# Kernel tuning notes

Hardware: AMD Instinct MI355X
Metric: run time of the kernel (lower is better)

The kernel has to match this reference:

```python
import jax, jax.numpy as jnp
import numpy as np
from jax import lax

B, C, H, W = 4, 128, 64, 64
GC = 32        # branch channels = C * branch_ratio
DI = 64        # SS2D d_inner = 2 * GC (expand=2)
DT_RANK = 2    # ceil(GC / 16)


def _conv(x, w, pad, dilation=1, groups=1):
    return lax.conv_general_dilated(x, w, (1, 1), [(pad, pad), (pad, pad)],
                                    rhs_dilation=(dilation, dilation),
                                    feature_group_count=groups,
                                    dimension_numbers=('NCHW', 'OIHW', 'NCHW'))


def _bn(x, g, b, m, v):
    # inference-mode BatchNorm2d
    s = g / jnp.sqrt(v + 1e-5)
    return x * s[None, :, None, None] + (b - m * s)[None, :, None, None]


def _selective_scan(u, delta, A, Bm, Cm, D, dbias):
    # u, delta: (B,K,Di,L); A: (K,Di,N); Bm,Cm: (B,K,N,L); D,dbias: (K,Di)
    delta = jax.nn.softplus(delta + dbias[None, :, :, None])
    Bsz, K, Di, L = u.shape
    N = A.shape[-1]

    def step(h, inp):
        dt, bt, ct, ut = inp  # dt,ut: (B,K,Di); bt,ct: (B,K,N)
        h = jnp.exp(dt[..., None] * A) * h + (dt * ut)[..., None] * bt[:, :, None, :]
        return h, jnp.einsum('bkdn,bkn->bkd', h, ct)

    xs = (jnp.moveaxis(delta, -1, 0), jnp.moveaxis(Bm, -1, 0),
          jnp.moveaxis(Cm, -1, 0), jnp.moveaxis(u, -1, 0))
    _, ys = lax.scan(step, jnp.zeros((Bsz, K, Di, N), u.dtype), xs)
    return jnp.moveaxis(ys, 0, -1) + u * D[None, :, :, None]


def _ss2d(x, in_w, cw, cb, xp_w, dt_w, dt_b, A_log, Dp, ln_g, ln_b, out_w):
    # VMamba SS2D on NCHW input
    Bsz, Cc, Hh, Ww = x.shape
    di = in_w.shape[0] // 2
    dc = cw.shape[-1]
    xz = jnp.einsum('bchw,ec->behw', x, in_w)          # in_proj (bias=False)
    xi, z = jnp.split(xz, 2, axis=1)
    xc = jax.nn.silu(_conv(xi, cw, (dc - 1) // 2, groups=di) + cb[None, :, None, None])
    L = Hh * Ww
    xf = xc.reshape(Bsz, di, L)
    xt = xc.transpose(0, 1, 3, 2).reshape(Bsz, di, L)
    x2 = jnp.stack([xf, xt], 1)
    xs4 = jnp.concatenate([x2, jnp.flip(x2, -1)], 1)   # (B,4,di,L) cross-scan
    x_dbl = jnp.einsum('bkdl,kcd->bkcl', xs4, xp_w)
    r = dt_w.shape[-1]
    N = A_log.shape[-1]
    dts = jnp.einsum('bkrl,kdr->bkdl', x_dbl[:, :, :r], dt_w)
    Bs = x_dbl[:, :, r:r + N]
    Cs = x_dbl[:, :, r + N:]
    A = -jnp.exp(A_log).reshape(4, di, N)
    oy = _selective_scan(xs4, dts, A, Bs, Cs, Dp.reshape(4, di), dt_b)
    inv = jnp.flip(oy[:, 2:4], -1)
    wh = oy[:, 1].reshape(Bsz, di, Ww, Hh).transpose(0, 1, 3, 2).reshape(Bsz, di, L)
    iwh = inv[:, 1].reshape(Bsz, di, Ww, Hh).transpose(0, 1, 3, 2).reshape(Bsz, di, L)
    y = (oy[:, 0] + inv[:, 0] + wh + iwh).transpose(0, 2, 1).reshape(Bsz, Hh, Ww, di)
    mu = y.mean(-1, keepdims=True)
    y = (y - mu) * lax.rsqrt(((y - mu) ** 2).mean(-1, keepdims=True) + 1e-5) * ln_g + ln_b
    y = y * jax.nn.silu(z.transpose(0, 2, 3, 1))
    return jnp.einsum('bhwd,cd->bchw', y, out_w)


def _gcss2d(x, in_w, cw, cb, xp_w, dt_w, dt_b, A_log, Dp, ln_g, ln_b, out_w, pw, bg, bb, bm, bv):
    s = _ss2d(x, in_w, cw, cb, xp_w, dt_w, dt_b, A_log, Dp, ln_g, ln_b, out_w)
    # AdaptiveAvgPool2d(1) + bilinear upsample of a 1x1 map == broadcast
    pool = jnp.broadcast_to(x.mean((2, 3), keepdims=True), s.shape)
    return jax.nn.relu(_bn(_conv(jnp.concatenate([s, pool], 1), pw, 0), bg, bb, bm, bv))


def _forward(x, conv1_w, conv1_bn_g, conv1_bn_b, conv1_bn_m, conv1_bn_v,
             ss2_in_proj_w, ss2_conv_w, ss2_conv_b, ss2_x_proj_w, ss2_dt_w, ss2_dt_b,
             ss2_A_log, ss2_D, ss2_ln_g, ss2_ln_b, ss2_out_proj_w,
             g2_proj_w, g2_bn_g, g2_bn_b, g2_bn_m, g2_bn_v,
             conv3_w,
             ss4_in_proj_w, ss4_conv_w, ss4_conv_b, ss4_x_proj_w, ss4_dt_w, ss4_dt_b,
             ss4_A_log, ss4_D, ss4_ln_g, ss4_ln_b, ss4_out_proj_w,
             g4_proj_w, g4_bn_g, g4_bn_b, g4_bn_m, g4_bn_v,
             gp_w, proj_w, proj_bn_g, proj_bn_b, proj_bn_m, proj_bn_v,
             ca_w1, ca_b1, ca_w2, ca_b2, sa_w):
    Cc = x.shape[1]
    x1, x2, x3, x4 = jnp.split(x, [Cc - 3 * GC, Cc - 2 * GC, Cc - GC], axis=1)
    out1 = jax.nn.relu(_bn(_conv(x1, conv1_w, 1), conv1_bn_g, conv1_bn_b, conv1_bn_m, conv1_bn_v))
    out2 = _gcss2d(x2, ss2_in_proj_w, ss2_conv_w, ss2_conv_b, ss2_x_proj_w, ss2_dt_w,
                   ss2_dt_b, ss2_A_log, ss2_D, ss2_ln_g, ss2_ln_b, ss2_out_proj_w,
                   g2_proj_w, g2_bn_g, g2_bn_b, g2_bn_m, g2_bn_v)
    out3 = jax.nn.relu(_conv(x3 + x1, conv3_w, 12, dilation=12))
    out4 = _gcss2d(x4 + x2, ss4_in_proj_w, ss4_conv_w, ss4_conv_b, ss4_x_proj_w, ss4_dt_w,
                   ss4_dt_b, ss4_A_log, ss4_D, ss4_ln_g, ss4_ln_b, ss4_out_proj_w,
                   g4_proj_w, g4_bn_g, g4_bn_b, g4_bn_m, g4_bn_v)
    fused = jnp.concatenate([out1, out2, out3, out4], 1)
    gf = jax.nn.relu(_conv(x.mean((2, 3), keepdims=True), gp_w, 0))
    gf = jnp.broadcast_to(gf, fused.shape)
    y = jnp.concatenate([fused, gf], 1)
    y = x + jax.nn.relu(_bn(_conv(y, proj_w, 0), proj_bn_g, proj_bn_b, proj_bn_m, proj_bn_v))
    # RCSA (dropout is identity in eval)
    ca = jax.nn.sigmoid(
        _conv(jax.nn.relu(_conv(y.mean((2, 3), keepdims=True), ca_w1, 0)
                          + ca_b1[None, :, None, None]), ca_w2, 0)
        + ca_b2[None, :, None, None])
    sa = jax.nn.sigmoid(_conv(y, sa_w, 3))
    return y * (ca * sa) + y


def setup_inputs():
    key = jax.random.key(0)
    ctr = [0]

    def rn(shape, s=0.1):
        ctr[0] += 1
        return s * jax.random.normal(jax.random.fold_in(key, ctr[0]), shape, jnp.float32)

    def alog(n):
        # VMamba A init: log(1..N) per (direction*d_inner) row
        return jnp.tile(jnp.log(jnp.arange(1, n + 1, dtype=jnp.float32))[None], (4 * DI, 1))

    return dict(
        x=rn((B, C, H, W), 1.0),
        conv1_w=rn((GC, GC, 3, 3)),
        conv1_bn_g=jnp.ones(GC), conv1_bn_b=jnp.zeros(GC),
        conv1_bn_m=jnp.zeros(GC), conv1_bn_v=jnp.ones(GC),
        ss2_in_proj_w=rn((2 * DI, GC)),
        ss2_conv_w=rn((DI, 1, 3, 3)), ss2_conv_b=rn((DI,)),
        ss2_x_proj_w=rn((4, DT_RANK + 2 * 8, DI)),
        ss2_dt_w=rn((4, DI, DT_RANK)), ss2_dt_b=rn((4, DI)),
        ss2_A_log=alog(8), ss2_D=jnp.ones(4 * DI),
        ss2_ln_g=jnp.ones(DI), ss2_ln_b=jnp.zeros(DI),
        ss2_out_proj_w=rn((GC, DI)),
        g2_proj_w=rn((GC, 2 * GC, 1, 1)),
        g2_bn_g=jnp.ones(GC), g2_bn_b=jnp.zeros(GC), g2_bn_m=jnp.zeros(GC), g2_bn_v=jnp.ones(GC),
        conv3_w=rn((GC, GC, 3, 3)),
        ss4_in_proj_w=rn((2 * DI, GC)),
        ss4_conv_w=rn((DI, 1, 7, 7)), ss4_conv_b=rn((DI,)),
        ss4_x_proj_w=rn((4, DT_RANK + 2 * 24, DI)),
        ss4_dt_w=rn((4, DI, DT_RANK)), ss4_dt_b=rn((4, DI)),
        ss4_A_log=alog(24), ss4_D=jnp.ones(4 * DI),
        ss4_ln_g=jnp.ones(DI), ss4_ln_b=jnp.zeros(DI),
        ss4_out_proj_w=rn((GC, DI)),
        g4_proj_w=rn((GC, 2 * GC, 1, 1)),
        g4_bn_g=jnp.ones(GC), g4_bn_b=jnp.zeros(GC), g4_bn_m=jnp.zeros(GC), g4_bn_v=jnp.ones(GC),
        gp_w=rn((C, C, 1, 1)),
        proj_w=rn((C, 2 * C, 1, 1)),
        proj_bn_g=jnp.ones(C), proj_bn_b=jnp.zeros(C),
        proj_bn_m=jnp.zeros(C), proj_bn_v=jnp.ones(C),
        ca_w1=rn((C // 16, C, 1, 1)), ca_b1=jnp.zeros(C // 16),
        ca_w2=rn((C, C // 16, 1, 1)), ca_b2=jnp.zeros(C),
        sa_w=rn((1, C, 7, 7)),
    )


def reference(x, conv1_w, conv1_bn_g, conv1_bn_b, conv1_bn_m, conv1_bn_v,
              ss2_in_proj_w, ss2_conv_w, ss2_conv_b, ss2_x_proj_w, ss2_dt_w, ss2_dt_b,
              ss2_A_log, ss2_D, ss2_ln_g, ss2_ln_b, ss2_out_proj_w,
              g2_proj_w, g2_bn_g, g2_bn_b, g2_bn_m, g2_bn_v,
              conv3_w,
              ss4_in_proj_w, ss4_conv_w, ss4_conv_b, ss4_x_proj_w, ss4_dt_w, ss4_dt_b,
              ss4_A_log, ss4_D, ss4_ln_g, ss4_ln_b, ss4_out_proj_w,
              g4_proj_w, g4_bn_g, g4_bn_b, g4_bn_m, g4_bn_v,
              gp_w, proj_w, proj_bn_g, proj_bn_b, proj_bn_m, proj_bn_v,
              ca_w1, ca_b1, ca_w2, ca_b2, sa_w):
    return _forward(x, conv1_w, conv1_bn_g, conv1_bn_b, conv1_bn_m, conv1_bn_v,
                    ss2_in_proj_w, ss2_conv_w, ss2_conv_b, ss2_x_proj_w, ss2_dt_w, ss2_dt_b,
                    ss2_A_log, ss2_D, ss2_ln_g, ss2_ln_b, ss2_out_proj_w,
                    g2_proj_w, g2_bn_g, g2_bn_b, g2_bn_m, g2_bn_v,
                    conv3_w,
                    ss4_in_proj_w, ss4_conv_w, ss4_conv_b, ss4_x_proj_w, ss4_dt_w, ss4_dt_b,
                    ss4_A_log, ss4_D, ss4_ln_g, ss4_ln_b, ss4_out_proj_w,
                    g4_proj_w, g4_bn_g, g4_bn_b, g4_bn_m, g4_bn_v,
                    gp_w, proj_w, proj_bn_g, proj_bn_b, proj_bn_m, proj_bn_v,
                    ca_w1, ca_b1, ca_w2, ca_b2, sa_w)
```

## Files before the change

kernel.cpp:

```cpp
#include <hip/hip_runtime.h>
#include <math.h>

#define BB 4
#define CCH 128
#define LL 4096
#define LOG2E 1.44269504088896340736f

__device__ __forceinline__ float exp2fast(float x) {
    float r; asm("v_exp_f32 %0, %1" : "=v"(r) : "v"(x)); return r;
}
__device__ __forceinline__ float softplusf(float x) {
    return x > 20.f ? x : log1pf(expf(x));
}
__device__ __forceinline__ float sigmf(float x) {
    return 1.f / (1.f + expf(-x));
}

__device__ __forceinline__ int dirmap(int k, int l) {
    if (k == 0) return l;
    if (k == 1) return ((l & 63) << 6) | (l >> 6);
    if (k == 2) return LL - 1 - l;
    int j = LL - 1 - l; return ((j & 63) << 6) | (j >> 6);
}

__global__ void k_prepA(const float* __restrict__ Alog2, const float* __restrict__ Alog4,
                        float* __restrict__ A2_2, float* __restrict__ A2_4) {
    int i = blockIdx.x * 256 + threadIdx.x;
    if (i < 4 * 64 * 8)  A2_2[i] = -expf(Alog2[i]) * LOG2E;
    if (i < 4 * 64 * 24) A2_4[i] = -expf(Alog4[i]) * LOG2E;
}

__global__ void k_addgroups(const float* __restrict__ x, float* __restrict__ x13, float* __restrict__ x42) {
    int i = blockIdx.x * 256 + threadIdx.x;
    int l = i & (LL - 1); int c = (i >> 12) & 31; int b = i >> 17;
    const float* xb = x + (size_t)b * CCH * LL;
    x13[i] = xb[(64 + c) * LL + l] + xb[(0 + c) * LL + l];
    x42[i] = xb[(96 + c) * LL + l] + xb[(32 + c) * LL + l];
}

__global__ void k_pool(const float* __restrict__ src, float* __restrict__ dst) {
    int bc = blockIdx.x;
    const float* p = src + (size_t)bc * LL;
    float s = 0.f;
    for (int i = threadIdx.x; i < LL; i += 256) s += p[i];
    for (int m = 32; m >= 1; m >>= 1) s += __shfl_xor(s, m, 64);
    __shared__ float ws[4];
    if ((threadIdx.x & 63) == 0) ws[threadIdx.x >> 6] = s;
    __syncthreads();
    if (threadIdx.x == 0) dst[bc] = (ws[0] + ws[1] + ws[2] + ws[3]) * (1.f / LL);
}

__global__ __launch_bounds__(256) void k_conv1L(const float* __restrict__ x,
                        const float* __restrict__ w1,
                        const float* __restrict__ g, const float* __restrict__ bt,
                        const float* __restrict__ m, const float* __restrict__ v,
                        float* __restrict__ out1) {
    __shared__ float t[32][3][66];
    int b = blockIdx.x >> 6, h = blockIdx.x & 63;
    int lane = threadIdx.x & 63, wv = threadIdx.x >> 6;
    const float* xb = x + (size_t)b * CCH * LL;
    for (int i = threadIdx.x; i < 192; i += 256) {
        int ci = i / 6, rem = i % 6;
        t[ci][rem >> 1][(rem & 1) ? 65 : 0] = 0.f;
    }
    for (int i = threadIdx.x; i < 6144; i += 256) {
        int ci = i / 192, rem = i % 192;
        int r = rem >> 6, col = rem & 63;
        int hh = h + r - 1;
        t[ci][r][col + 1] = ((unsigned)hh < 64u) ? xb[ci * LL + hh * 64 + col] : 0.f;
    }
    __syncthreads();
    float a[8];
    #pragma unroll
    for (int j = 0; j < 8; j++) a[j] = 0.f;
    for (int ci = 0; ci < 32; ci++) {
        #pragma unroll
        for (int r = 0; r < 3; r++) {
            float v0 = t[ci][r][lane];
            float v1 = t[ci][r][lane + 1];
            float v2 = t[ci][r][lane + 2];
            #pragma unroll
            for (int j = 0; j < 8; j++) {
                const float* wp = w1 + ((wv * 8 + j) * 32 + ci) * 9 + r * 3;
                a[j] = fmaf(wp[0], v0, fmaf(wp[1], v1, fmaf(wp[2], v2, a[j])));
            }
        }
    }
    #pragma unroll
    for (int j = 0; j < 8; j++) {
        int co = wv * 8 + j;
        float sc = g[co] * rsqrtf(v[co] + 1e-5f);
        float bs = bt[co] - m[co] * sc;
        out1[(size_t)(b * 32 + co) * LL + h * 64 + lane] = fmaxf(fmaf(a[j], sc, bs), 0.f);
    }
}

__global__ __launch_bounds__(256) void k_conv3L(const float* __restrict__ x13,
                        const float* __restrict__ w3, float* __restrict__ out3) {
    __shared__ float t[32][3][88];
    int b = blockIdx.x >> 6, h = blockIdx.x & 63;
    int lane = threadIdx.x & 63, wv = threadIdx.x >> 6;
    const float* xb = x13 + (size_t)b * 32 * LL;
    for (int i = threadIdx.x; i < 2304; i += 256) {
        int ci = i / 72, rem = i % 72;
        int r = rem / 24, cz = rem % 24;
        t[ci][r][(cz < 12) ? cz : (cz + 64)] = 0.f;
    }
    for (int i = threadIdx.x; i < 6144; i += 256) {
        int ci = i / 192, rem = i % 192;
        int r = rem >> 6, col = rem & 63;
        int hh = h + (r - 1) * 12;
        t[ci][r][col + 12] = ((unsigned)hh < 64u) ? xb[ci * LL + hh * 64 + col] : 0.f;
    }
    __syncthreads();
    float a[8];
    #pragma unroll
    for (int j = 0; j < 8; j++) a[j] = 0.f;
    for (int ci = 0; ci < 32; ci++) {
        #pragma unroll
        for (int r = 0; r < 3; r++) {
            float v0 = t[ci][r][lane];
            float v1 = t[ci][r][lane + 12];
            float v2 = t[ci][r][lane + 24];
            #pragma unroll
            for (int j = 0; j < 8; j++) {
                const float* wp = w3 + ((wv * 8 + j) * 32 + ci) * 9 + r * 3;
                a[j] = fmaf(wp[0], v0, fmaf(wp[1], v1, fmaf(wp[2], v2, a[j])));
            }
        }
    }
    #pragma unroll
    for (int j = 0; j < 8; j++) {
        int co = wv * 8 + j;
        out3[(size_t)(b * 32 + co) * LL + h * 64 + lane] = fmaxf(a[j], 0.f);
    }
}

__global__ __launch_bounds__(256) void k_s1(const float* __restrict__ src, int bstride, int coff,
                     const float* __restrict__ in_w,
                     float* __restrict__ xiT, float* __restrict__ zT) {
    int blk = blockIdx.x;
    int l0 = (blk & 63) * 64; int b = blk >> 6;
    int lq = threadIdx.x & 63; int esub = threadIdx.x >> 6;
    __shared__ float xin[32][64];
    __shared__ float xit[64][65];
    __shared__ float zt[64][65];
    for (int i = threadIdx.x; i < 32 * 64; i += 256) {
        int c = i >> 6, q = i & 63;
        xin[c][q] = src[(size_t)b * bstride + (size_t)(coff + c) * LL + l0 + q];
    }
    __syncthreads();
    for (int it = 0; it < 32; it++) {
        int e = esub * 32 + it;
        const float* wr = in_w + e * 32;
        float acc = 0.f;
        #pragma unroll 8
        for (int c = 0; c < 32; c++) acc += wr[c] * xin[c][lq];
        if (e < 64) xit[lq][e] = acc;
        else        zt[lq][e - 64] = acc;
    }
    __syncthreads();
    for (int i = threadIdx.x; i < 64 * 64; i += 256) {
        int q = i >> 6, d = i & 63;
        size_t st = ((size_t)b * LL + l0 + q) * 64 + d;
        xiT[st] = xit[q][d];
        zT[st]  = zt[q][d];
    }
}

template<int K>
__global__ __launch_bounds__(256) void k_s2(const float* __restrict__ xiT, const float* __restrict__ cw,
                     const float* __restrict__ cb, float* __restrict__ xcT) {
    __shared__ float wl[64 * K * K];
    for (int j = threadIdx.x; j < 64 * K * K; j += 256) wl[j] = cw[j];
    __syncthreads();
    int i = blockIdx.x * 256 + threadIdx.x;
    int d = i & 63; int l = (i >> 6) & (LL - 1); int b = i >> 18;
    int h = l >> 6, wx = l & 63;
    const int P = (K - 1) / 2;
    const float* xb = xiT + (size_t)b * LL * 64;
    const float* wp = wl + d * K * K;
    float acc = cb[d];
    #pragma unroll
    for (int kh = 0; kh < K; kh++) {
        int hh = h + kh - P; if ((unsigned)hh >= 64u) continue;
        #pragma unroll
        for (int kw = 0; kw < K; kw++) {
            int w2 = wx + kw - P; if ((unsigned)w2 >= 64u) continue;
            acc += wp[kh * K + kw] * xb[(size_t)(hh * 64 + w2) * 64 + d];
        }
    }
    xcT[i] = acc / (1.f + expf(-acc));
}

template<int N>
__global__ __launch_bounds__(256) void k_s3(const float* __restrict__ xcT, const float* __restrict__ xp_w,
                     float* __restrict__ r01, float* __restrict__ Bsb, float* __restrict__ Csb) {
    const int CD = 2 + 2 * N;
    int blk = blockIdx.x;
    int lt = blk & 255; int k = (blk >> 8) & 3; int b = blk >> 10;
    int l0 = lt * 16; int bk = b * 4 + k;
    __shared__ float xt[64][17];
    __shared__ float xp[CD * 64];
    __shared__ float accs[CD][16];
    for (int i = threadIdx.x; i < 64 * 16; i += 256) {
        int dd = i & 63, lq = i >> 6;
        xt[dd][lq] = xcT[((size_t)b * LL + dirmap(k, l0 + lq)) * 64 + dd];
    }
    for (int i = threadIdx.x; i < CD * 64; i += 256) xp[i] = xp_w[(size_t)k * CD * 64 + i];
    __syncthreads();
    for (int o = threadIdx.x; o < CD * 16; o += 256) {
        int cc = o >> 4, lq = o & 15;
        const float* wr = &xp[cc * 64];
        float acc = 0.f;
        #pragma unroll 8
        for (int dd = 0; dd < 64; dd++) acc += wr[dd] * xt[dd][lq];
        accs[cc][lq] = acc;
    }
    __syncthreads();
    for (int i = threadIdx.x; i < 32; i += 256) {
        int lq = i >> 1, j = i & 1;
        r01[((size_t)bk * LL + l0 + lq) * 2 + j] = accs[j][lq];
    }
    for (int i = threadIdx.x; i < 16 * N; i += 256) {
        int lq = i / N, n = i - lq * N;
        Bsb[((size_t)bk * LL + l0 + lq) * N + n] = accs[2 + n][lq];
        Csb[((size_t)bk * LL + l0 + lq) * N + n] = accs[2 + N + n][lq];
    }
}

template<int N>
__global__ __launch_bounds__(256) void k_scanA(
    const float* __restrict__ r01, const float* __restrict__ Bs,
    const float* __restrict__ xcT, const float* __restrict__ A2,
    const float* __restrict__ dtw, const float* __restrict__ dtb,
    float* __restrict__ Pp, float* __restrict__ Hl) {
    int bk = blockIdx.x >> 5; int c = (blockIdx.x & 31) * 4 + (threadIdx.x >> 6);
    int d = threadIdx.x & 63;
    int k = bk & 3, b = bk >> 2;
    float w0 = dtw[(k * 64 + d) * 2], w1 = dtw[(k * 64 + d) * 2 + 1], bd = dtb[k * 64 + d];
    float a2[N], h[N], P[N];
    #pragma unroll
    for (int n = 0; n < N; n++) { a2[n] = A2[(k * 64 + d) * N + n]; h[n] = 0.f; P[n] = 1.f; }
    const float2* rp  = (const float2*)(r01 + (size_t)bk * LL * 2);
    const float4* Bp4 = (const float4*)(Bs + (size_t)bk * LL * N);
    const float*  xb  = xcT + (size_t)b * LL * 64;
    int l0 = c * 32;
    for (int t = 0; t < 32; t++) {
        int l = l0 + t;
        float2 rv = rp[l];
        float dt = softplusf(fmaf(rv.x, w0, fmaf(rv.y, w1, bd)));
        float du = dt * xb[(size_t)dirmap(k, l) * 64 + d];
        #pragma unroll
        for (int n4 = 0; n4 < N / 4; n4++) {
            float4 bv = Bp4[(size_t)l * (N / 4) + n4];
            float bvs[4] = {bv.x, bv.y, bv.z, bv.w};
            #pragma unroll
            for (int j = 0; j < 4; j++) {
                int n = n4 * 4 + j;
                float a = exp2fast(dt * a2[n]);
                P[n] *= a;
                h[n] = fmaf(a, h[n], du * bvs[j]);
            }
        }
    }
    size_t o = (size_t)(bk * 128 + c) * N * 64 + d;
    #pragma unroll
    for (int n = 0; n < N; n++) { Pp[o + n * 64] = P[n]; Hl[o + n * 64] = h[n]; }
}

template<int N>
__global__ void k_scanB(const float* __restrict__ Pp, float* __restrict__ Hl) {
    int g = blockIdx.x * 256 + threadIdx.x;
    if (g >= 16 * N * 64) return;
    int d = g & 63; int n = (g >> 6) % N; int bk = g / (N * 64);
    float acc = 0.f;
    for (int c = 0; c < 128; c++) {
        size_t o = (size_t)(bk * 128 + c) * N * 64 + n * 64 + d;
        float Pv = Pp[o], Hv = Hl[o];
        Hl[o] = acc;
        acc = fmaf(Pv, acc, Hv);
    }
}

template<int N>
__global__ __launch_bounds__(256) void k_scanC(
    const float* __restrict__ r01, const float* __restrict__ Bs,
    const float* __restrict__ Cs, const float* __restrict__ xcT,
    const float* __restrict__ A2, const float* __restrict__ dtw,
    const float* __restrict__ dtb, const float* __restrict__ Hin,
    float* __restrict__ yrT) {
    int bk = blockIdx.x >> 5; int c = (blockIdx.x & 31) * 4 + (threadIdx.x >> 6);
    int d = threadIdx.x & 63;
    int k = bk & 3, b = bk >> 2;
    float w0 = dtw[(k * 64 + d) * 2], w1 = dtw[(k * 64 + d) * 2 + 1], bd = dtb[k * 64 + d];
    float a2[N], h[N];
    size_t o = (size_t)(bk * 128 + c) * N * 64 + d;
    #pragma unroll
    for (int n = 0; n < N; n++) { a2[n] = A2[(k * 64 + d) * N + n]; h[n] = Hin[o + n * 64]; }
    const float2* rp  = (const float2*)(r01 + (size_t)bk * LL * 2);
    const float4* Bp4 = (const float4*)(Bs + (size_t)bk * LL * N);
    const float4* Cp4 = (const float4*)(Cs + (size_t)bk * LL * N);
    const float*  xb  = xcT + (size_t)b * LL * 64;
    float* yo = yrT + (size_t)(k * BB + b) * LL * 64 + d;
    int l0 = c * 32;
    for (int t = 0; t < 32; t++) {
        int l = l0 + t;
        float2 rv = rp[l];
        float dt = softplusf(fmaf(rv.x, w0, fmaf(rv.y, w1, bd)));
        int lm = dirmap(k, l);
        float du = dt * xb[(size_t)lm * 64 + d];
        float y = 0.f;
        #pragma unroll
        for (int n4 = 0; n4 < N / 4; n4++) {
            float4 bv = Bp4[(size_t)l * (N / 4) + n4];
            float4 cv = Cp4[(size_t)l * (N / 4) + n4];
            float bvs[4] = {bv.x, bv.y, bv.z, bv.w};
            float cvs[4] = {cv.x, cv.y, cv.z, cv.w};
            #pragma unroll
            for (int j = 0; j < 4; j++) {
                int n = n4 * 4 + j;
                float a = exp2fast(dt * a2[n]);
                h[n] = fmaf(a, h[n], du * bvs[j]);
                y = fmaf(h[n], cvs[j], y);
            }
        }
        yo[(size_t)lm * 64] = y;
    }
}

__global__ __launch_bounds__(256) void k_combine(const float* __restrict__ yrT, const float* __restrict__ xcT,
                          const float* __restrict__ zT, const float* __restrict__ Dp,
                          const float* __restrict__ ln_g, const float* __restrict__ ln_b,
                          const float* __restrict__ out_w, float* __restrict__ sbuf) {
    int blk = blockIdx.x;
    int l0 = (blk & 127) * 32; int b = blk >> 7;
    int tid = threadIdx.x;
    __shared__ float yt[32][65];
    __shared__ float yg[32][65];
    __shared__ float muS[32], rsS[32];
    const size_t DS = (size_t)BB * LL * 64;
    for (int i = tid; i < 2048; i += 256) {
        int d = i & 63, q = i >> 6;
        size_t st = ((size_t)b * LL + l0 + q) * 64 + d;
        float yv = yrT[st] + yrT[DS + st] + yrT[2 * DS + st] + yrT[3 * DS + st];
        float sd = Dp[d] + Dp[64 + d] + Dp[128 + d] + Dp[192 + d];
        yt[q][d] = fmaf(xcT[st], sd, yv);
    }
    __syncthreads();
    {
        int q = tid >> 3, sub = tid & 7;
        float s = 0.f, sq = 0.f;
        #pragma unroll
        for (int j = 0; j < 8; j++) {
            float vv = yt[q][sub * 8 + j]; s += vv; sq = fmaf(vv, vv, sq);
        }
        #pragma unroll
        for (int m = 1; m < 8; m <<= 1) {
            s += __shfl_xor(s, m, 64); sq += __shfl_xor(sq, m, 64);
        }
        if (sub == 0) {
            float mm = s * (1.f / 64.f);
            muS[q] = mm;
            rsS[q] = rsqrtf(fmaf(sq, 1.f / 64.f, -mm * mm) + 1e-5f);
        }
    }
    __syncthreads();
    for (int i = tid; i < 2048; i += 256) {
        int d = i & 63, q = i >> 6;
        float gn = fmaf((yt[q][d] - muS[q]) * rsS[q], ln_g[d], ln_b[d]);
        float z = zT[((size_t)b * LL + l0 + q) * 64 + d];
        yg[q][d] = gn * z / (1.f + expf(-z));
    }
    __syncthreads();
    for (int i = tid; i < 32 * 32; i += 256) {
        int e = i >> 5, q = i & 31;
        const float* wr = out_w + e * 64;
        float acc = 0.f;
        #pragma unroll 8
        for (int d = 0; d < 64; d++) acc += wr[d] * yg[q][d];
        sbuf[((size_t)b * 32 + e) * LL + l0 + q] = acc;
    }
}

__global__ __launch_bounds__(256) void k_gtail(const float* __restrict__ sbuf, const float* __restrict__ pw,
                        const float* __restrict__ gfpool, int poolOff, int poolOff2,
                        const float* __restrict__ g, const float* __restrict__ bt,
                        const float* __restrict__ m, const float* __restrict__ v,
                        float* __restrict__ out) {
    int i = blockIdx.x * 256 + threadIdx.x;
    int l4 = i & 1023; int co = (i >> 10) & 31; int b = i >> 15;
    int l = l4 << 2;
    const float* pwr = pw + co * 64;
    float pacc = 0.f;
    #pragma unroll 8
    for (int c = 0; c < 32; c++) {
        float pv = gfpool[b * 128 + poolOff + c];
        if (poolOff2 >= 0) pv += gfpool[b * 128 + poolOff2 + c];
        pacc = fmaf(pwr[32 + c], pv, pacc);
    }
    float a0 = pacc, a1 = pacc, a2 = pacc, a3 = pacc;
    const float* sb = sbuf + (size_t)b * 32 * LL + l;
    #pragma unroll 8
    for (int c = 0; c < 32; c++) {
        float4 sv = *(const float4*)(sb + (size_t)c * LL);
        float wk = pwr[c];
        a0 = fmaf(wk, sv.x, a0);
        a1 = fmaf(wk, sv.y, a1);
        a2 = fmaf(wk, sv.z, a2);
        a3 = fmaf(wk, sv.w, a3);
    }
    float sc = g[co] * rsqrtf(v[co] + 1e-5f);
    float bs = bt[co] - m[co] * sc;
    float4 o;
    o.x = fmaxf(fmaf(a0, sc, bs), 0.f);
    o.y = fmaxf(fmaf(a1, sc, bs), 0.f);
    o.z = fmaxf(fmaf(a2, sc, bs), 0.f);
    o.w = fmaxf(fmaf(a3, sc, bs), 0.f);
    *(float4*)(out + (size_t)(b * 32 + co) * LL + l) = o;
}

__global__ void k_gf(const float* __restrict__ gfpool, const float* __restrict__ gp_w,
                     const float* __restrict__ proj_w, float* __restrict__ gf, float* __restrict__ pgf) {
    __shared__ float gfl[4][128];
    int t = threadIdx.x;
    int b = t >> 7, e = t & 127;
    float acc = 0.f;
    for (int c = 0; c < 128; c++) acc += gp_w[e * 128 + c] * gfpool[b * 128 + c];
    acc = fmaxf(acc, 0.f);
    gf[b * 128 + e] = acc; gfl[b][e] = acc;
    __syncthreads();
    float a2 = 0.f;
    for (int c = 0; c < 128; c++) a2 += proj_w[e * 256 + 128 + c] * gfl[b][c];
    pgf[b * 128 + e] = a2;
}

__global__ __launch_bounds__(256) void k_proj(const float* __restrict__ x,
                       const float* __restrict__ o1, const float* __restrict__ o2,
                       const float* __restrict__ o3, const float* __restrict__ o4,
                       const float* __restrict__ proj_w, const float* __restrict__ pgf,
                       const float* __restrict__ g, const float* __restrict__ bt,
                       const float* __restrict__ m, const float* __restrict__ v,
                       float* __restrict__ ybuf) {
    int i = blockIdx.x * 256 + threadIdx.x;
    int l4 = i & 1023; int co = (i >> 10) & 127; int b = i >> 17;
    int l = l4 << 2;
    const float* wr = proj_w + co * 256;
    float pg = pgf[b * 128 + co];
    float a0 = pg, a1 = pg, a2 = pg, a3 = pg;
    size_t ob = (size_t)b * 32 * LL + l;
    #pragma unroll 8
    for (int c = 0; c < 32; c++) {
        float4 vv = *(const float4*)(o1 + ob + (size_t)c * LL);
        float wk = wr[c];
        a0 = fmaf(wk, vv.x, a0); a1 = fmaf(wk, vv.y, a1);
        a2 = fmaf(wk, vv.z, a2); a3 = fmaf(wk, vv.w, a3);
    }
    #pragma unroll 8
    for (int c = 0; c < 32; c++) {
        float4 vv = *(const float4*)(o2 + ob + (size_t)c * LL);
        float wk = wr[32 + c];
        a0 = fmaf(wk, vv.x, a0); a1 = fmaf(wk, vv.y, a1);
        a2 = fmaf(wk, vv.z, a2); a3 = fmaf(wk, vv.w, a3);
    }
    #pragma unroll 8
    for (int c = 0; c < 32; c++) {
        float4 vv = *(const float4*)(o3 + ob + (size_t)c * LL);
        float wk = wr[64 + c];
        a0 = fmaf(wk, vv.x, a0); a1 = fmaf(wk, vv.y, a1);
        a2 = fmaf(wk, vv.z, a2); a3 = fmaf(wk, vv.w, a3);
    }
    #pragma unroll 8
    for (int c = 0; c < 32; c++) {
        float4 vv = *(const float4*)(o4 + ob + (size_t)c * LL);
        float wk = wr[96 + c];
        a0 = fmaf(wk, vv.x, a0); a1 = fmaf(wk, vv.y, a1);
        a2 = fmaf(wk, vv.z, a2); a3 = fmaf(wk, vv.w, a3);
    }
    float sc = g[co] * rsqrtf(v[co] + 1e-5f);
    float bs = bt[co] - m[co] * sc;
    float4 xv = *(const float4*)(x + (size_t)(b * 128 + co) * LL + l);
    float4 o;
    o.x = xv.x + fmaxf(fmaf(a0, sc, bs), 0.f);
    o.y = xv.y + fmaxf(fmaf(a1, sc, bs), 0.f);
    o.z = xv.z + fmaxf(fmaf(a2, sc, bs), 0.f);
    o.w = xv.w + fmaxf(fmaf(a3, sc, bs), 0.f);
    *(float4*)(ybuf + (size_t)(b * 128 + co) * LL + l) = o;
}

__global__ void k_ca(const float* __restrict__ ypool, const float* __restrict__ w1,
                     const float* __restrict__ b1, const float* __restrict__ w2,
                     const float* __restrict__ b2, float* __restrict__ ca) {
    int b = blockIdx.x; int t = threadIdx.x;
    __shared__ float ym[128]; __shared__ float r1[8];
    ym[t] = ypool[b * 128 + t];
    __syncthreads();
    if (t < 8) {
        float a = b1[t];
        for (int c = 0; c < 128; c++) a += w1[t * 128 + c] * ym[c];
        r1[t] = fmaxf(a, 0.f);
    }
    __syncthreads();
    float a = b2[t];
    #pragma unroll
    for (int i2 = 0; i2 < 8; i2++) a += w2[t * 8 + i2] * r1[i2];
    ca[b * 128 + t] = sigmf(a);
}

__global__ __launch_bounds__(256) void k_sa_part(const float* __restrict__ ybuf, const float* __restrict__ sw,
                     float* __restrict__ pa) {
    __shared__ float wlds[16 * 49];
    __shared__ float rows[4][7][70];
    __shared__ float part[4][64];
    int cg = blockIdx.x & 7; int h = (blockIdx.x >> 3) & 63; int b = blockIdx.x >> 9;
    int lane = threadIdx.x & 63, wv = threadIdx.x >> 6;
    for (int i = threadIdx.x; i < 16 * 49; i += 256) wlds[i] = sw[cg * 16 * 49 + i];
    if (lane < 3) {
        #pragma unroll
        for (int r = 0; r < 7; r++) { rows[wv][r][lane] = 0.f; rows[wv][r][67 + lane] = 0.f; }
    }
    __syncthreads();
    float acc = 0.f;
    for (int it = 0; it < 4; it++) {
        int lc = it * 4 + wv; int c = cg * 16 + lc;
        const float* yp = ybuf + ((size_t)b * 128 + c) * LL;
        #pragma unroll
        for (int r = 0; r < 7; r++) {
            int hh = h + r - 3;
            rows[wv][r][3 + lane] = ((unsigned)hh < 64u) ? yp[hh * 64 + lane] : 0.f;
        }
        __syncthreads();
        const float* wp = wlds + lc * 49;
        #pragma unroll
        for (int kh = 0; kh < 7; kh++) {
            #pragma unroll
            for (int kw = 0; kw < 7; kw++) {
                acc = fmaf(wp[kh * 7 + kw], rows[wv][kh][lane + kw], acc);
            }
        }
        __syncthreads();
    }
    part[wv][lane] = acc;
    __syncthreads();
    if (threadIdx.x < 64) {
        float a = part[0][threadIdx.x] + part[1][threadIdx.x]
                + part[2][threadIdx.x] + part[3][threadIdx.x];
        pa[(size_t)cg * (BB * LL) + (size_t)b * LL + h * 64 + threadIdx.x] = a;
    }
}

__global__ void k_sared(const float* __restrict__ pa, float* __restrict__ sa) {
    int i = blockIdx.x * 256 + threadIdx.x;
    float s = 0.f;
    #pragma unroll
    for (int g = 0; g < 8; g++) s += pa[(size_t)g * (BB * LL) + i];
    sa[i] = sigmf(s);
}

__global__ void k_final(const float* __restrict__ ybuf, const float* __restrict__ ca,
                        const float* __restrict__ sa, float* __restrict__ out) {
    int i = blockIdx.x * 256 + threadIdx.x;
    int l = i & (LL - 1); int co = (i >> 12) & 127; int b = i >> 19;
    float y = ybuf[i];
    out[i] = y * (1.f + ca[b * 128 + co] * sa[b * 4096 + l]);
}

extern "C" void kernel_launch(void* const* d_in, const int* in_sizes, int n_in,
                              void* d_out, int out_size, void* d_ws, size_t ws_size,
                              hipStream_t stream) {
    const float* x        = (const float*)d_in[0];
    const float* conv1_w  = (const float*)d_in[1];
    const float* c1g = (const float*)d_in[2], *c1b = (const float*)d_in[3];
    const float* c1m = (const float*)d_in[4], *c1v = (const float*)d_in[5];
    const float* s2_inw   = (const float*)d_in[6];
    const float* s2_cw    = (const float*)d_in[7];
    const float* s2_cb    = (const float*)d_in[8];
    const float* s2_xpw   = (const float*)d_in[9];
    const float* s2_dtw   = (const float*)d_in[10];
    const float* s2_dtb   = (const float*)d_in[11];
    const float* s2_Alog  = (const float*)d_in[12];
    const float* s2_D     = (const float*)d_in[13];
    const float* s2_lng   = (const float*)d_in[14];
    const float* s2_lnb   = (const float*)d_in[15];
    const float* s2_outw  = (const float*)d_in[16];
    const float* g2_pw    = (const float*)d_in[17];
    const float* g2g = (const float*)d_in[18], *g2b = (const float*)d_in[19];
    const float* g2m = (const float*)d_in[20], *g2v = (const float*)d_in[21];
    const float* conv3_w  = (const float*)d_in[22];
    const float* s4_inw   = (const float*)d_in[23];
    const float* s4_cw    = (const float*)d_in[24];
    const float* s4_cb    = (const float*)d_in[25];
    const float* s4_xpw   = (const float*)d_in[26];
    const float* s4_dtw   = (const float*)d_in[27];
    const float* s4_dtb   = (const float*)d_in[28];
    const float* s4_Alog  = (const float*)d_in[29];
    const float* s4_D     = (const float*)d_in[30];
    const float* s4_lng   = (const float*)d_in[31];
    const float* s4_lnb   = (const float*)d_in[32];
    const float* s4_outw  = (const float*)d_in[33];
    const float* g4_pw    = (const float*)d_in[34];
    const float* g4g = (const float*)d_in[35], *g4b = (const float*)d_in[36];
    const float* g4m = (const float*)d_in[37], *g4v = (const float*)d_in[38];
    const float* gp_w     = (const float*)d_in[39];
    const float* proj_w   = (const float*)d_in[40];
    const float* pjg = (const float*)d_in[41], *pjb = (const float*)d_in[42];
    const float* pjm = (const float*)d_in[43], *pjv = (const float*)d_in[44];
    const float* ca_w1 = (const float*)d_in[45], *ca_b1 = (const float*)d_in[46];
    const float* ca_w2 = (const float*)d_in[47], *ca_b2 = (const float*)d_in[48];
    const float* sa_w  = (const float*)d_in[49];
    float* out = (float*)d_out;
    float* w = (float*)d_ws;

    const size_t o_out1 = 0;
    const size_t o_out2 = 524288;
    const size_t o_out3 = 1048576;
    const size_t o_out4 = 1572864;
    const size_t o_x42  = 2097152;
    const size_t o_gfp  = 2621440;
    const size_t o_gf   = 2621952;
    const size_t o_pgf  = 2622464;
    const size_t o_ypool= 2622976;
    const size_t o_ca   = 2623488;
    const size_t o_A2   = 2624000;
    const size_t o_A4   = 2626048;
    const size_t o_S    = 2632192;
    const size_t o_x13  = o_S;
    const size_t o_xiT  = o_S;
    const size_t o_Pp   = o_S;
    const size_t o_yrT  = o_S;
    const size_t o_ybuf = o_S;
    const size_t o_sa   = o_S + 2097152;
    const size_t o_sap  = o_S + 2113536;
    const size_t o_zT   = o_S + 4194304;
    const size_t o_xcT  = o_zT + 1048576;
    const size_t o_r01  = o_xcT + 1048576;
    const size_t o_Bs   = o_r01 + 131072;
    const size_t o_sbuf = o_Bs;
    const size_t o_Cs   = o_Bs + 1572864;
    const size_t o_Hl   = o_Cs + 1572864;

    dim3 b256(256);
    k_prepA<<<24, b256, 0, stream>>>(s2_Alog, s4_Alog, w + o_A2, w + o_A4);
    k_addgroups<<<2048, b256, 0, stream>>>(x, w + o_x13, w + o_x42);
    k_pool<<<512, b256, 0, stream>>>(x, w + o_gfp);
    k_conv1L<<<256, b256, 0, stream>>>(x, conv1_w, c1g, c1b, c1m, c1v, w + o_out1);
    k_conv3L<<<256, b256, 0, stream>>>(w + o_x13, conv3_w, w + o_out3);

    {
        const int N = 8;
        k_s1<<<256, b256, 0, stream>>>(x, CCH * LL, 32, s2_inw, w + o_xiT, w + o_zT);
        k_s2<3><<<4096, b256, 0, stream>>>(w + o_xiT, s2_cw, s2_cb, w + o_xcT);
        k_s3<N><<<4096, b256, 0, stream>>>(w + o_xcT, s2_xpw, w + o_r01, w + o_Bs, w + o_Cs);
        k_scanA<N><<<512, b256, 0, stream>>>(w + o_r01, w + o_Bs, w + o_xcT, w + o_A2,
                                             s2_dtw, s2_dtb, w + o_Pp, w + o_Hl);
        k_scanB<N><<<(16 * N * 64 + 255) / 256, b256, 0, stream>>>(w + o_Pp, w + o_Hl);
        k_scanC<N><<<512, b256, 0, stream>>>(w + o_r01, w + o_Bs, w + o_Cs, w + o_xcT,
                                             w + o_A2, s2_dtw, s2_dtb, w + o_Hl, w + o_yrT);
        k_combine<<<512, b256, 0, stream>>>(w + o_yrT, w + o_xcT, w + o_zT, s2_D,
                                            s2_lng, s2_lnb, s2_outw, w + o_sbuf);
        k_gtail<<<512, b256, 0, stream>>>(w + o_sbuf, g2_pw, w + o_gfp, 32, -1,
                                          g2g, g2b, g2m, g2v, w + o_out2);
    }
    {
        const int N = 24;
        k_s1<<<256, b256, 0, stream>>>(w + o_x42, 32 * LL, 0, s4_inw, w + o_xiT, w + o_zT);
        k_s2<7><<<4096, b256, 0, stream>>>(w + o_xiT, s4_cw, s4_cb, w + o_xcT);
        k_s3<N><<<4096, b256, 0, stream>>>(w + o_xcT, s4_xpw, w + o_r01, w + o_Bs, w + o_Cs);
        k_scanA<N><<<512, b256, 0, stream>>>(w + o_r01, w + o_Bs, w + o_xcT, w + o_A4,
                                             s4_dtw, s4_dtb, w + o_Pp, w + o_Hl);
        k_scanB<N><<<(16 * N * 64 + 255) / 256, b256, 0, stream>>>(w + o_Pp, w + o_Hl);
        k_scanC<N><<<512, b256, 0, stream>>>(w + o_r01, w + o_Bs, w + o_Cs, w + o_xcT,
                                             w + o_A4, s4_dtw, s4_dtb, w + o_Hl, w + o_yrT);
        k_combine<<<512, b256, 0, stream>>>(w + o_yrT, w + o_xcT, w + o_zT, s4_D,
                                            s4_lng, s4_lnb, s4_outw, w + o_sbuf);
        k_gtail<<<512, b256, 0, stream>>>(w + o_sbuf, g4_pw, w + o_gfp, 96, 32,
                                          g4g, g4b, g4m, g4v, w + o_out4);
    }

    k_gf<<<1, dim3(512), 0, stream>>>(w + o_gfp, gp_w, proj_w, w + o_gf, w + o_pgf);
    k_proj<<<2048, b256, 0, stream>>>(x, w + o_out1, w + o_out2, w + o_out3, w + o_out4,
                                      proj_w, w + o_pgf, pjg, pjb, pjm, pjv, w + o_ybuf);
    k_pool<<<512, b256, 0, stream>>>(w + o_ybuf, w + o_ypool);
    k_ca<<<4, dim3(128), 0, stream>>>(w + o_ypool, ca_w1, ca_b1, ca_w2, ca_b2, w + o_ca);
    k_sa_part<<<2048, b256, 0, stream>>>(w + o_ybuf, sa_w, w + o_sap);
    k_sared<<<64, b256, 0, stream>>>(w + o_sap, w + o_sa);
    k_final<<<8192, b256, 0, stream>>>(w + o_ybuf, w + o_ca, w + o_sa, out);
}
```

Before: 697.0 us.

## Split scan state dimension across waves and stage B/C/dt in shared memory

The chunked selective-scan kernels now give each block a single 32-step chunk and split the N state dimension across the four waves, each handling N/4 states. The grid therefore grows fourfold and per-thread register arrays shrink. Softplus of dt and dt*u are computed once per chunk into shared memory, and B/C rows are staged in LDS. Partial y sums are reduced across waves through shared memory before the global store. The carry-propagation kernel also prefetches the next chunk's values. The cost is extra barriers and LDS traffic in exchange for more parallelism and occupancy.

```diff
diff --git a/kernel.cpp b/kernel.cpp
--- a/kernel.cpp
+++ b/kernel.cpp
@@ -235,38 +235,52 @@
     const float* __restrict__ xcT, const float* __restrict__ A2,
     const float* __restrict__ dtw, const float* __restrict__ dtb,
     float* __restrict__ Pp, float* __restrict__ Hl) {
-    int bk = blockIdx.x >> 5; int c = (blockIdx.x & 31) * 4 + (threadIdx.x >> 6);
-    int d = threadIdx.x & 63;
+    const int N4 = N / 4;
+    __shared__ float2 dd2[32][64];
+    __shared__ float lb[32 * N];
+    int bk = blockIdx.x >> 7; int c = blockIdx.x & 127;
     int k = bk & 3, b = bk >> 2;
-    float w0 = dtw[(k * 64 + d) * 2], w1 = dtw[(k * 64 + d) * 2 + 1], bd = dtb[k * 64 + d];
-    float a2[N], h[N], P[N];
-    #pragma unroll
-    for (int n = 0; n < N; n++) { a2[n] = A2[(k * 64 + d) * N + n]; h[n] = 0.f; P[n] = 1.f; }
-    const float2* rp  = (const float2*)(r01 + (size_t)bk * LL * 2);
-    const float4* Bp4 = (const float4*)(Bs + (size_t)bk * LL * N);
-    const float*  xb  = xcT + (size_t)b * LL * 64;
+    int tid = threadIdx.x;
+    int d = tid & 63, wv = tid >> 6;
     int l0 = c * 32;
+    const float* Bp = Bs + ((size_t)bk * LL + l0) * N;
+    for (int i = tid; i < 32 * N; i += 256) lb[i] = Bp[i];
+    {
+        float w0 = dtw[(k * 64 + d) * 2], w1 = dtw[(k * 64 + d) * 2 + 1], bd = dtb[k * 64 + d];
+        const float2* rp = (const float2*)(r01 + (size_t)bk * LL * 2);
+        const float* xb = xcT + (size_t)b * LL * 64;
+        #pragma unroll
+        for (int j = 0; j < 8; j++) {
+            int t = wv * 8 + j;
+            float2 rv = rp[l0 + t];
+            float u = xb[(size_t)dirmap(k, l0 + t) * 64 + d];
+            float dt = softplusf(fmaf(rv.x, w0, fmaf(rv.y, w1, bd)));
+            dd2[t][d] = make_float2(dt, dt * u);
+        }
+    }
+    __syncthreads();
+    float a2[N4], h[N4], P[N4];
+    #pragma unroll
+    for (int n = 0; n < N4; n++) {
+        a2[n] = A2[(k * 64 + d) * N + wv * N4 + n];
+        h[n] = 0.f; P[n] = 1.f;
+    }
     for (int t = 0; t < 32; t++) {
-        int l = l0 + t;
-        float2 rv = rp[l];
-        float dt = softplusf(fmaf(rv.x, w0, fmaf(rv.y, w1, bd)));
-        float du = dt * xb[(size_t)dirmap(k, l) * 64 + d];
-        #pragma unroll
-        for (int n4 = 0; n4 < N / 4; n4++) {
-            float4 bv = Bp4[(size_t)l * (N / 4) + n4];
-            float bvs[4] = {bv.x, bv.y, bv.z, bv.w};
-            #pragma unroll
-            for (int j = 0; j < 4; j++) {
-                int n = n4 * 4 + j;
-                float a = exp2fast(dt * a2[n]);
-                P[n] *= a;
-                h[n] = fmaf(a, h[n], du * bvs[j]);
-            }
+        float2 dv = dd2[t][d];
+        const float* bl = &lb[t * N + wv * N4];
+        #pragma unroll
+        for (int n = 0; n < N4; n++) {
+            float a = exp2fast(dv.x * a2[n]);
+            P[n] *= a;
+            h[n] = fmaf(a, h[n], dv.y * bl[n]);
         }
     }
     size_t o = (size_t)(bk * 128 + c) * N * 64 + d;
     #pragma unroll
-    for (int n = 0; n < N; n++) { Pp[o + n * 64] = P[n]; Hl[o + n * 64] = h[n]; }
+    for (int n = 0; n < N4; n++) {
+        Pp[o + (size_t)(wv * N4 + n) * 64] = P[n];
+        Hl[o + (size_t)(wv * N4 + n) * 64] = h[n];
+    }
 }
 
 template<int N>
@@ -274,12 +288,17 @@
     int g = blockIdx.x * 256 + threadIdx.x;
     if (g >= 16 * N * 64) return;
     int d = g & 63; int n = (g >> 6) % N; int bk = g / (N * 64);
+    const size_t stride = (size_t)N * 64;
+    size_t o = (size_t)bk * 128 * stride + n * 64 + d;
     float acc = 0.f;
+    float Pv = Pp[o], Hv = Hl[o];
     for (int c = 0; c < 128; c++) {
-        size_t o = (size_t)(bk * 128 + c) * N * 64 + n * 64 + d;
-        float Pv = Pp[o], Hv = Hl[o];
+        float Pn = 0.f, Hn = 0.f;
+        if (c < 127) { Pn = Pp[o + stride]; Hn = Hl[o + stride]; }
         Hl[o] = acc;
         acc = fmaf(Pv, acc, Hv);
+        Pv = Pn; Hv = Hn;
+        o += stride;
     }
 }
 
@@ -290,42 +309,64 @@
     const float* __restrict__ A2, const float* __restrict__ dtw,
     const float* __restrict__ dtb, const float* __restrict__ Hin,
     float* __restrict__ yrT) {
-    int bk = blockIdx.x >> 5; int c = (blockIdx.x & 31) * 4 + (threadIdx.x >> 6);
-    int d = threadIdx.x & 63;
+    const int N4 = N / 4;
+    __shared__ float2 dd2[32][64];
+    __shared__ float lb[32 * N];
+    __shared__ float lc[32 * N];
+    __shared__ float yacc[4][8][64];
+    int bk = blockIdx.x >> 7; int c = blockIdx.x & 127;
     int k = bk & 3, b = bk >> 2;
-    float w0 = dtw[(k * 64 + d) * 2], w1 = dtw[(k * 64 + d) * 2 + 1], bd = dtb[k * 64 + d];
-    float a2[N], h[N];
+    int tid = threadIdx.x;
+    int d = tid & 63, wv = tid >> 6;
+    int l0 = c * 32;
+    const float* Bp = Bs + ((size_t)bk * LL + l0) * N;
+    const float* Cp = Cs + ((size_t)bk * LL + l0) * N;
+    for (int i = tid; i < 32 * N; i += 256) { lb[i] = Bp[i]; lc[i] = Cp[i]; }
+    {
+        float w0 = dtw[(k * 64 + d) * 2], w1 = dtw[(k * 64 + d) * 2 + 1], bd = dtb[k * 64 + d];
+        const float2* rp = (const float2*)(r01 + (size_t)bk * LL * 2);
+        const float* xb = xcT + (size_t)b * LL * 64;
+        #pragma unroll
+        for (int j = 0; j < 8; j++) {
+            int t = wv * 8 + j;
+            float2 rv = rp[l0 + t];
+            float u = xb[(size_t)dirmap(k, l0 + t) * 64 + d];
+            float dt = softplusf(fmaf(rv.x, w0, fmaf(rv.y, w1, bd)));
+            dd2[t][d] = make_float2(dt, dt * u);
+        }
+    }
+    float a2[N4], h[N4];
     size_t o = (size_t)(bk * 128 + c) * N * 64 + d;
     #pragma unroll
-    for (int n = 0; n < N; n++) { a2[n] = A2[(k * 64 + d) * N + n]; h[n] = Hin[o + n * 64]; }
-    const float2* rp  = (const float2*)(r01 + (size_t)bk * LL * 2);
-    const float4* Bp4 = (const float4*)(Bs + (size_t)bk * LL * N);
-    const float4* Cp4 = (const float4*)(Cs + (size_t)bk * LL * N);
-    const float*  xb  = xcT + (size_t)b * LL * 64;
-    float* yo = yrT + (size_t)(k * BB + b) * LL * 64 + d;
-    int l0 = c * 32;
-    for (int t = 0; t < 32; t++) {
-        int l = l0 + t;
-        float2 rv = rp[l];
-        float dt = softplusf(fmaf(rv.x, w0, fmaf(rv.y, w1, bd)));
-        int lm = dirmap(k, l);
-        float du = dt * xb[(size_t)lm * 64 + d];
-        float y = 0.f;
-        #pragma unroll
-        for (int n4 = 0; n4 < N / 4; n4++) {
-            float4 bv = Bp4[(size_t)l * (N / 4) + n4];
-            float4 cv = Cp4[(size_t)l * (N / 4) + n4];
-            float bvs[4] = {bv.x, bv.y, bv.z, bv.w};
-            float cvs[4] = {cv.x, cv.y, cv.z, cv.w};
+    for (int n = 0; n < N4; n++) {
+        a2[n] = A2[(k * 64 + d) * N + wv * N4 + n];
+        h[n] = Hin[o + (size_t)(wv * N4 + n) * 64];
+    }
+    __syncthreads();
+    float* yo = yrT + (size_t)(k * BB + b) * LL * 64;
+    for (int st = 0; st < 4; st++) {
+        #pragma unroll
+        for (int j = 0; j < 8; j++) {
+            int t = st * 8 + j;
+            float2 dv = dd2[t][d];
+            const float* bl = &lb[t * N + wv * N4];
+            const float* cl = &lc[t * N + wv * N4];
+            float y = 0.f;
             #pragma unroll
-            for (int j = 0; j < 4; j++) {
-                int n = n4 * 4 + j;
-                float a = exp2fast(dt * a2[n]);
-                h[n] = fmaf(a, h[n], du * bvs[j]);
-                y = fmaf(h[n], cvs[j], y);
+            for (int n = 0; n < N4; n++) {
+                float a = exp2fast(dv.x * a2[n]);
+                h[n] = fmaf(a, h[n], dv.y * bl[n]);
+                y = fmaf(h[n], cl[n], y);
             }
-        }
-        yo[(size_t)lm * 64] = y;
+            yacc[wv][j][d] = y;
+        }
+        __syncthreads();
+        for (int i = tid; i < 512; i += 256) {
+            int j = i >> 6, q = i & 63;
+            float y = yacc[0][j][q] + yacc[1][j][q] + yacc[2][j][q] + yacc[3][j][q];
+            yo[(size_t)dirmap(k, l0 + st * 8 + j) * 64 + q] = y;
+        }
+        __syncthreads();
     }
 }
 
@@ -651,11 +692,11 @@
         k_s1<<<256, b256, 0, stream>>>(x, CCH * LL, 32, s2_inw, w + o_xiT, w + o_zT);
         k_s2<3><<<4096, b256, 0, stream>>>(w + o_xiT, s2_cw, s2_cb, w + o_xcT);
         k_s3<N><<<4096, b256, 0, stream>>>(w + o_xcT, s2_xpw, w + o_r01, w + o_Bs, w + o_Cs);
-        k_scanA<N><<<512, b256, 0, stream>>>(w + o_r01, w + o_Bs, w + o_xcT, w + o_A2,
-                                             s2_dtw, s2_dtb, w + o_Pp, w + o_Hl);
+        k_scanA<N><<<2048, b256, 0, stream>>>(w + o_r01, w + o_Bs, w + o_xcT, w + o_A2,
+                                              s2_dtw, s2_dtb, w + o_Pp, w + o_Hl);
         k_scanB<N><<<(16 * N * 64 + 255) / 256, b256, 0, stream>>>(w + o_Pp, w + o_Hl);
-        k_scanC<N><<<512, b256, 0, stream>>>(w + o_r01, w + o_Bs, w + o_Cs, w + o_xcT,
-                                             w + o_A2, s2_dtw, s2_dtb, w + o_Hl, w + o_yrT);
+        k_scanC<N><<<2048, b256, 0, stream>>>(w + o_r01, w + o_Bs, w + o_Cs, w + o_xcT,
+                                              w + o_A2, s2_dtw, s2_dtb, w + o_Hl, w + o_yrT);
         k_combine<<<512, b256, 0, stream>>>(w + o_yrT, w + o_xcT, w + o_zT, s2_D,
                                             s2_lng, s2_lnb, s2_outw, w + o_sbuf);
         k_gtail<<<512, b256, 0, stream>>>(w + o_sbuf, g2_pw, w + o_gfp, 32, -1,
@@ -666,11 +707,11 @@
         k_s1<<<256, b256, 0, stream>>>(w + o_x42, 32 * LL, 0, s4_inw, w + o_xiT, w + o_zT);
         k_s2<7><<<4096, b256, 0, stream>>>(w + o_xiT, s4_cw, s4_cb, w + o_xcT);
         k_s3<N><<<4096, b256, 0, stream>>>(w + o_xcT, s4_xpw, w + o_r01, w + o_Bs, w + o_Cs);
-        k_scanA<N><<<512, b256, 0, stream>>>(w + o_r01, w + o_Bs, w + o_xcT, w + o_A4,
-                                             s4_dtw, s4_dtb, w + o_Pp, w + o_Hl);
+        k_scanA<N><<<2048, b256, 0, stream>>>(w + o_r01, w + o_Bs, w + o_xcT, w + o_A4,
+                                              s4_dtw, s4_dtb, w + o_Pp, w + o_Hl);
         k_scanB<N><<<(16 * N * 64 + 255) / 256, b256, 0, stream>>>(w + o_Pp, w + o_Hl);
-        k_scanC<N><<<512, b256, 0, stream>>>(w + o_r01, w + o_Bs, w + o_Cs, w + o_xcT,
-                                             w + o_A4, s4_dtw, s4_dtb, w + o_Hl, w + o_yrT);
+        k_scanC<N><<<2048, b256, 0, stream>>>(w + o_r01, w + o_Bs, w + o_Cs, w + o_xcT,
+                                              w + o_A4, s4_dtw, s4_dtb, w + o_Hl, w + o_yrT);
         k_combine<<<512, b256, 0, stream>>>(w + o_yrT, w + o_xcT, w + o_zT, s4_D,
                                             s4_lng, s4_lnb, s4_outw, w + o_sbuf);
         k_gtail<<<512, b256, 0, stream>>>(w + o_sbuf, g4_pw, w + o_gfp, 96, 32,
```

After: 624.4 us. -10.4%, faster.
